# Kernel optimization log

Measured on AMD Instinct MI355X. Metric: run time of the kernel, lower is better.

The kernel has to match this reference:

```python
import jax, jax.numpy as jnp
import numpy as np

N_NODES = 100000
NEG_SLOPE = 0.2  # PyG GATConv default


def gat_conv(x, src, dst, W, a_src, a_dst, n_nodes):
    """One PyG-style GATConv (with self-loops already appended to src/dst).
    x: [N, Fin], W: [Fin, H*C], a_src/a_dst: [H, C]. Returns [N, H, C]."""
    H, C = a_src.shape
    h = (x @ W).reshape(-1, H, C)                      # [N, H, C]
    s_src = jnp.einsum('nhc,hc->nh', h, a_src)         # [N, H]
    s_dst = jnp.einsum('nhc,hc->nh', h, a_dst)         # [N, H]
    e = jax.nn.leaky_relu(s_src[src] + s_dst[dst], NEG_SLOPE)  # [E, H]
    # segment softmax over incoming edges of each destination node
    e_max = jax.ops.segment_max(e, dst, num_segments=n_nodes)  # [N, H]
    e_exp = jnp.exp(e - e_max[dst])
    denom = jax.ops.segment_sum(e_exp, dst, num_segments=n_nodes)
    alpha = e_exp / (denom[dst] + 1e-16)               # [E, H]
    msg = h[src] * alpha[:, :, None]                   # [E, H, C]
    return jax.ops.segment_sum(msg, dst, num_segments=n_nodes)  # [N, H, C]


def setup_inputs() -> dict:
    key = jax.random.key(0)
    ks = jax.random.split(key, 10)
    in_dim, hidden, heads, out_dim = 128, 32, 4, 32
    N, E = N_NODES, 1600000
    x = jax.random.normal(ks[0], (N, in_dim), dtype=jnp.float32)
    edge_index = jax.random.randint(ks[1], (2, E), 0, N, dtype=jnp.int64)
    s = 0.1
    return {
        'x': x,
        'edge_index': edge_index,
        'W1': s * jax.random.normal(ks[2], (in_dim, heads * hidden), dtype=jnp.float32),
        'a_src1': s * jax.random.normal(ks[3], (heads, hidden), dtype=jnp.float32),
        'a_dst1': s * jax.random.normal(ks[4], (heads, hidden), dtype=jnp.float32),
        'b1': jnp.zeros((heads * hidden,), dtype=jnp.float32),
        'W2': s * jax.random.normal(ks[5], (heads * hidden, out_dim), dtype=jnp.float32),
        'a_src2': s * jax.random.normal(ks[6], (1, out_dim), dtype=jnp.float32),
        'a_dst2': s * jax.random.normal(ks[7], (1, out_dim), dtype=jnp.float32),
        'b2': jnp.zeros((out_dim,), dtype=jnp.float32),
    }


def reference(x, edge_index, W1, a_src1, a_dst1, b1, W2, a_src2, a_dst2, b2):
    N = x.shape[0]
    loops = jnp.arange(N, dtype=edge_index.dtype)
    src = jnp.concatenate([edge_index[0], loops])  # PyG adds self-loops
    dst = jnp.concatenate([edge_index[1], loops])
    h1 = gat_conv(x, src, dst, W1, a_src1, a_dst1, N)      # [N, H, C]
    h1 = jax.nn.elu(h1.reshape(N, -1) + b1)                # concat heads + bias, elu
    h2 = gat_conv(h1, src, dst, W2, a_src2, a_dst2, N)     # [N, 1, out]
    return h2.mean(axis=1) + b2                            # concat=False -> mean over heads
```

## Files before the change

kernel.cpp:

```cpp
#include <hip/hip_runtime.h>
#include <hip/hip_bf16.h>

#define NEG 0.2f
#define BK_SHIFT 9
#define BK_CAP 9216

typedef short short8 __attribute__((ext_vector_type(8)));
typedef float f32x4 __attribute__((ext_vector_type(4)));

__device__ __forceinline__ float lrelu(float x){ return x > 0.f ? x : NEG * x; }
__device__ __forceinline__ float elu_fast(float x){ return x > 0.f ? x : __expf(x) - 1.f; }
__device__ __forceinline__ unsigned short f2bf(float f){
  unsigned int u = __float_as_uint(f);
  unsigned int r = u + 0x7fffu + ((u >> 16) & 1u);
  return (unsigned short)(r >> 16);
}
__device__ __forceinline__ float bf2f(unsigned short u){
  return __uint_as_float(((unsigned int)u) << 16);
}
__device__ __forceinline__ float2 bfu2(unsigned int v){
  float2 r;
  r.x = __uint_as_float(v << 16);
  r.y = __uint_as_float(v & 0xffff0000u);
  return r;
}

#define EB_SRC_MASK 0x7fffffu

__global__ __launch_bounds__(512) void k_binA_packW(
    const int* __restrict__ src, const int* __restrict__ dst, int E,
    int* __restrict__ gcursor, unsigned int* __restrict__ ebuf,
    const float* __restrict__ W, unsigned short* __restrict__ Wp,
    const float* __restrict__ W2, unsigned short* __restrict__ Wp2, int nA){
  __shared__ int hist[256];
  __shared__ int base[256];
  int t = threadIdx.x;
  int bid = blockIdx.x;
  if (bid >= nA){
    int idx = (bid - nA) * 512 + t;
    if (idx < 16384){
      int n = idx >> 7, k = idx & 127;
      Wp[n * 128 + k] = f2bf(W[(size_t)k * 128 + n]);
    } else {
      int i2 = idx - 16384;
      int n = i2 >> 7, k = i2 & 127;
      Wp2[n * 128 + k] = f2bf(W2[(size_t)k * 32 + n]);
    }
    return;
  }
  if (t < 256) hist[t] = 0;
  __syncthreads();
  int e0 = bid * 4096;
  int dsr[8], ssr[8];
  #pragma unroll
  for (int j = 0; j < 8; j++){
    int e = e0 + j * 512 + t;
    if (e < E){
      dsr[j] = dst[e]; ssr[j] = src[e];
      atomicAdd(&hist[dsr[j] >> BK_SHIFT], 1);
    } else dsr[j] = -1;
  }
  __syncthreads();
  if (t < 256){
    int cnt = hist[t];
    if (cnt > 0) base[t] = atomicAdd(&gcursor[t], cnt);
    hist[t] = 0;
  }
  __syncthreads();
  #pragma unroll
  for (int j = 0; j < 8; j++){
    if (dsr[j] >= 0){
      int d = dsr[j]; int b = d >> BK_SHIFT;
      int loc = atomicAdd(&hist[b], 1);
      unsigned int dloc = (unsigned int)(d & ((1 << BK_SHIFT) - 1));
      ebuf[(size_t)b * BK_CAP + base[b] + loc] = (unsigned int)ssr[j] | (dloc << 23);
    }
  }
}

__global__ __launch_bounds__(256, 3) void k_csrC_gemm1(
    const unsigned int* __restrict__ ebuf, const int* __restrict__ gcount,
    int* __restrict__ rowp, int* __restrict__ csr, int N, int NBK, int total,
    const float* __restrict__ x, const unsigned short* __restrict__ Wp,
    const float* __restrict__ a_src, const float* __restrict__ a_dst,
    unsigned short* __restrict__ h_bf, float* __restrict__ ss, float* __restrict__ sd){
  __shared__ __align__(16) unsigned short Wt[128 * 136];
  __shared__ __align__(16) unsigned short Xb[64 * 136];
  int t = threadIdx.x;

  if (blockIdx.x < (unsigned)NBK){
    int* hist = (int*)Wt;
    int* psum = hist + 512;
    int* bsum = psum + 256;
    int b = blockIdx.x;
    int nbase = b << BK_SHIFT;
    int cnt = gcount[b];
    const unsigned int* eb = ebuf + (size_t)b * BK_CAP;
    hist[t] = 0; hist[t + 256] = 0;
    int bv = 0;
    {
      int nodes = 0;
      if (t < NBK){ int nb = N - (t << BK_SHIFT); nodes = nb > 512 ? 512 : nb; bv = gcount[t] + nodes; }
      bsum[t] = bv;
    }
    __syncthreads();
    for (int off = 1; off < 256; off <<= 1){
      int xv = (t >= off) ? bsum[t - off] : 0;
      __syncthreads();
      bsum[t] += xv;
      __syncthreads();
    }
    for (int i = t; i < cnt; i += 256)
      atomicAdd(&hist[eb[i] >> 23], 1);
    __syncthreads();
    int v0 = hist[2 * t], v1 = hist[2 * t + 1];
    int ps = v0 + v1;
    psum[t] = ps;
    __syncthreads();
    for (int off = 1; off < 256; off <<= 1){
      int xv = (t >= off) ? psum[t - off] : 0;
      __syncthreads();
      psum[t] += xv;
      __syncthreads();
    }
    {
      int eo = psum[t] - ps;
      int bb = (b == 0) ? 0 : bsum[b - 1];
      int n0 = 2 * t, n1 = 2 * t + 1;
      int r0 = bb + eo + n0;
      int r1 = bb + eo + v0 + n1;
      if (nbase + n0 < N) rowp[nbase + n0] = r0;
      if (nbase + n1 < N) rowp[nbase + n1] = r1;
      hist[n0] = r0; hist[n1] = r1;
    }
    if (b == 0 && t == 0) rowp[N] = total;
    __syncthreads();
    for (int i = t; i < cnt; i += 256){
      unsigned int e = eb[i];
      int pos = atomicAdd(&hist[e >> 23], 1);
      csr[pos] = (int)(e & EB_SRC_MASK);
    }
    __syncthreads();
    {
      int n0 = 2 * t, n1 = 2 * t + 1;
      if (nbase + n0 < N) csr[hist[n0]] = nbase + n0;
      if (nbase + n1 < N) csr[hist[n1]] = nbase + n1;
    }
    return;
  }

  int rb = (blockIdx.x - NBK) * 64;

  #pragma unroll
  for (int j = 0; j < 8; j++){
    int fi = j * 256 + t;
    int n = fi >> 4, ch = fi & 15;
    *(uint4*)&Wt[n * 136 + ch * 8] = *(const uint4*)&Wp[n * 128 + ch * 8];
  }
  #pragma unroll
  for (int j = 0; j < 8; j++){
    int fi = j * 256 + t;
    int row = fi >> 5, k4 = (fi & 31) * 4;
    int gr = rb + row;
    float4 v = make_float4(0.f, 0.f, 0.f, 0.f);
    if (gr < N) v = *(const float4*)&x[(size_t)gr * 128 + k4];
    uint2 pk;
    pk.x = ((unsigned)f2bf(v.y) << 16) | f2bf(v.x);
    pk.y = ((unsigned)f2bf(v.w) << 16) | f2bf(v.z);
    *(uint2*)&Xb[row * 136 + k4] = pk;
  }
  __syncthreads();

  int w = t >> 6, l = t & 63;
  int m = l & 15, quad = l >> 4;
  f32x4 acc[8];
  #pragma unroll
  for (int ct = 0; ct < 8; ct++) acc[ct] = (f32x4){0.f, 0.f, 0.f, 0.f};

  #pragma unroll
  for (int kc = 0; kc < 4; kc++){
    short8 a = *(const short8*)&Xb[(w * 16 + m) * 136 + kc * 32 + quad * 8];
    #pragma unroll
    for (int ct = 0; ct < 8; ct++){
      short8 bfr = *(const short8*)&Wt[(ct * 16 + m) * 136 + kc * 32 + quad * 8];
      acc[ct] = __builtin_amdgcn_mfma_f32_16x16x32_bf16(a, bfr, acc[ct], 0, 0, 0);
    }
  }

  float as[8], ad[8];
  #pragma unroll
  for (int ct = 0; ct < 8; ct++){ as[ct] = a_src[ct * 16 + m]; ad[ct] = a_dst[ct * 16 + m]; }

  #pragma unroll
  for (int reg = 0; reg < 4; reg++){
    int gr = rb + w * 16 + quad * 4 + reg;
    bool ok = gr < N;
    if (ok){
      #pragma unroll
      for (int ct = 0; ct < 8; ct++)
        h_bf[(size_t)gr * 128 + ct * 16 + m] = f2bf(acc[ct][reg]);
    }
    #pragma unroll
    for (int hh = 0; hh < 4; hh++){
      float pss = acc[2*hh][reg] * as[2*hh] + acc[2*hh+1][reg] * as[2*hh+1];
      float pd = acc[2*hh][reg] * ad[2*hh] + acc[2*hh+1][reg] * ad[2*hh+1];
      pss += __shfl_xor(pss, 1, 16); pss += __shfl_xor(pss, 2, 16);
      pss += __shfl_xor(pss, 4, 16); pss += __shfl_xor(pss, 8, 16);
      pd += __shfl_xor(pd, 1, 16); pd += __shfl_xor(pd, 2, 16);
      pd += __shfl_xor(pd, 4, 16); pd += __shfl_xor(pd, 8, 16);
      if (m == 0 && ok){ ss[(size_t)gr * 4 + hh] = pss; sd[(size_t)gr * 4 + hh] = pd; }
    }
  }
}

__global__ __launch_bounds__(256) void k_agg1(
    const int* __restrict__ row_ptr, const int* __restrict__ csr_src,
    const float* __restrict__ ss, const float* __restrict__ sdst,
    const unsigned short* __restrict__ hb,
    unsigned int* __restrict__ out1_bf, int N){
  int n = blockIdx.x * 4 + (threadIdx.x >> 6);
  if (n >= N) return;
  int l = threadIdx.x & 63;
  int q  = (l & 7) + ((l >> 5) << 3);
  int hh = (l >> 3) & 3;
  int slot = l >> 4;
  int c = l & 15;
  int hd = c >> 2;
  float sdw = sdst[(size_t)n * 4 + hh];
  int beg = row_ptr[n], end = row_ptr[n + 1];

  float acc[8] = {0.f,0.f,0.f,0.f,0.f,0.f,0.f,0.f};
  float swacc = 0.f;

  int e = beg;
  int remaining = end - beg;
  int qc = q < remaining ? q : 0;
  int sj = csr_src[e + qc];
  float sv = ss[(size_t)sj * 4 + hh];

  while (remaining > 0){
    int cur = remaining > 16 ? 16 : remaining;
    float wv = (q < cur) ? __expf(lrelu(sv + sdw)) : 0.f;
    swacc += wv;
    int sjc = sj;
    int rn = remaining - 16;
    if (rn > 0){
      int qn = q < rn ? q : 0;
      sj = csr_src[e + 16 + qn];
      sv = ss[(size_t)sj * 4 + hh];
    }
    #pragma unroll
    for (int p = 0; p < 4; p++){
      int base_p = ((p & 1) << 2) + ((p >> 1) << 3);
      if (base_p < cur){
        int sl = ((p & 1) << 2) + slot + ((p >> 1) << 5);
        int s  = __shfl(sjc, sl, 64);
        float w = __shfl(wv, sl + (hd << 3), 64);
        uint4 u = *(const uint4*)&hb[(size_t)s * 128 + (c << 3)];
        float2 f0 = bfu2(u.x), f1 = bfu2(u.y), f2 = bfu2(u.z), f3 = bfu2(u.w);
        acc[0] += w * f0.x; acc[1] += w * f0.y;
        acc[2] += w * f1.x; acc[3] += w * f1.y;
        acc[4] += w * f2.x; acc[5] += w * f2.y;
        acc[6] += w * f3.x; acc[7] += w * f3.y;
      }
    }
    e += 16; remaining = rn;
  }

  #pragma unroll
  for (int i = 0; i < 8; i++){
    acc[i] += __shfl_xor(acc[i], 16, 64);
    acc[i] += __shfl_xor(acc[i], 32, 64);
  }
  swacc += __shfl_xor(swacc, 1, 64);
  swacc += __shfl_xor(swacc, 2, 64);
  swacc += __shfl_xor(swacc, 4, 64);
  swacc += __shfl_xor(swacc, 32, 64);
  float sw = __shfl(swacc, hd << 3, 64);
  float inv = 1.f / (sw + 1e-16f);
  if (slot == 0){
    unsigned int o0 = ((unsigned)f2bf(acc[1] * inv) << 16) | f2bf(acc[0] * inv);
    unsigned int o1 = ((unsigned)f2bf(acc[3] * inv) << 16) | f2bf(acc[2] * inv);
    unsigned int o2 = ((unsigned)f2bf(acc[5] * inv) << 16) | f2bf(acc[4] * inv);
    unsigned int o3 = ((unsigned)f2bf(acc[7] * inv) << 16) | f2bf(acc[6] * inv);
    uint4 o; o.x = o0; o.y = o1; o.z = o2; o.w = o3;
    *(uint4*)&out1_bf[(size_t)n * 64 + (c << 2)] = o;
  }
}

__global__ __launch_bounds__(256) void k_gemm2m(
    const unsigned int* __restrict__ out1_bf, const float* __restrict__ b1,
    const unsigned short* __restrict__ Wp2,
    const float* __restrict__ a_src, const float* __restrict__ a_dst,
    unsigned short* __restrict__ h2_bf, float* __restrict__ ss2, float* __restrict__ sd2, int N){
  __shared__ __align__(16) unsigned short Wt[32 * 136];
  __shared__ __align__(16) unsigned short Xb[128 * 136];
  int t = threadIdx.x;
  int rb = blockIdx.x * 128;

  #pragma unroll
  for (int j = 0; j < 2; j++){
    int fi = j * 256 + t;
    int n = fi >> 4, ch = fi & 15;
    *(uint4*)&Wt[n * 136 + ch * 8] = *(const uint4*)&Wp2[n * 128 + ch * 8];
  }
  #pragma unroll
  for (int j = 0; j < 8; j++){
    int fi = j * 256 + t;
    int row = fi >> 4, qq = fi & 15;
    int gr = rb + row;
    uint4 o = make_uint4(0u, 0u, 0u, 0u);
    if (gr < N){
      uint4 u = *(const uint4*)&out1_bf[(size_t)gr * 64 + qq * 4];
      float4 bva = *(const float4*)&b1[qq * 8];
      float4 bvb = *(const float4*)&b1[qq * 8 + 4];
      float v0 = elu_fast(bf2f((unsigned short)(u.x & 0xffff)) + bva.x);
      float v1 = elu_fast(bf2f((unsigned short)(u.x >> 16))    + bva.y);
      float v2 = elu_fast(bf2f((unsigned short)(u.y & 0xffff)) + bva.z);
      float v3 = elu_fast(bf2f((unsigned short)(u.y >> 16))    + bva.w);
      float v4 = elu_fast(bf2f((unsigned short)(u.z & 0xffff)) + bvb.x);
      float v5 = elu_fast(bf2f((unsigned short)(u.z >> 16))    + bvb.y);
      float v6 = elu_fast(bf2f((unsigned short)(u.w & 0xffff)) + bvb.z);
      float v7 = elu_fast(bf2f((unsigned short)(u.w >> 16))    + bvb.w);
      o.x = ((unsigned)f2bf(v1) << 16) | f2bf(v0);
      o.y = ((unsigned)f2bf(v3) << 16) | f2bf(v2);
      o.z = ((unsigned)f2bf(v5) << 16) | f2bf(v4);
      o.w = ((unsigned)f2bf(v7) << 16) | f2bf(v6);
    }
    *(uint4*)&Xb[row * 136 + qq * 8] = o;
  }
  __syncthreads();

  int w = t >> 6, l = t & 63;
  int m = l & 15, quad = l >> 4;
  f32x4 acc[2][2];
  #pragma unroll
  for (int rg = 0; rg < 2; rg++){
    acc[rg][0] = (f32x4){0.f, 0.f, 0.f, 0.f};
    acc[rg][1] = (f32x4){0.f, 0.f, 0.f, 0.f};
  }

  #pragma unroll
  for (int kc = 0; kc < 4; kc++){
    #pragma unroll
    for (int ct = 0; ct < 2; ct++){
      short8 bfr = *(const short8*)&Wt[(ct * 16 + m) * 136 + kc * 32 + quad * 8];
      #pragma unroll
      for (int rg = 0; rg < 2; rg++){
        short8 a = *(const short8*)&Xb[(rg * 64 + w * 16 + m) * 136 + kc * 32 + quad * 8];
        acc[rg][ct] = __builtin_amdgcn_mfma_f32_16x16x32_bf16(a, bfr, acc[rg][ct], 0, 0, 0);
      }
    }
  }

  float as0 = a_src[m], as1 = a_src[16 + m];
  float ad0 = a_dst[m], ad1 = a_dst[16 + m];

  #pragma unroll
  for (int rg = 0; rg < 2; rg++){
    #pragma unroll
    for (int reg = 0; reg < 4; reg++){
      int gr = rb + rg * 64 + w * 16 + quad * 4 + reg;
      bool ok = gr < N;
      if (ok){
        h2_bf[(size_t)gr * 32 + m]      = f2bf(acc[rg][0][reg]);
        h2_bf[(size_t)gr * 32 + 16 + m] = f2bf(acc[rg][1][reg]);
      }
      float ps = acc[rg][0][reg] * as0 + acc[rg][1][reg] * as1;
      float pd = acc[rg][0][reg] * ad0 + acc[rg][1][reg] * ad1;
      ps += __shfl_xor(ps, 1, 16); ps += __shfl_xor(ps, 2, 16);
      ps += __shfl_xor(ps, 4, 16); ps += __shfl_xor(ps, 8, 16);
      pd += __shfl_xor(pd, 1, 16); pd += __shfl_xor(pd, 2, 16);
      pd += __shfl_xor(pd, 4, 16); pd += __shfl_xor(pd, 8, 16);
      if (m == 0 && ok){ ss2[gr] = ps; sd2[gr] = pd; }
    }
  }
}

__global__ __launch_bounds__(256) void k_agg2(
    const int* __restrict__ row_ptr, const int* __restrict__ csr_src,
    const float* __restrict__ ss2, const float* __restrict__ sd2,
    const unsigned short* __restrict__ h2bf, const float* __restrict__ b2,
    float* __restrict__ out, int N){
  int n = blockIdx.x * 4 + (threadIdx.x >> 6);
  if (n >= N) return;
  int l = threadIdx.x & 63;
  int q = l & 31;
  int slot = l >> 2;
  int ch4 = l & 3;
  float sdv = sd2[n];
  int beg = row_ptr[n], end = row_ptr[n + 1];

  float acc[8] = {0.f,0.f,0.f,0.f,0.f,0.f,0.f,0.f};
  float swacc = 0.f;

  int e = beg;
  int remaining = end - beg;
  int qc = q < remaining ? q : 0;
  int sj = csr_src[e + qc];
  float sv = ss2[sj];

  while (remaining > 0){
    int cur = remaining > 32 ? 32 : remaining;
    float wv = (q < cur) ? __expf(lrelu(sv + sdv)) : 0.f;
    swacc += wv;
    int sjc = sj; float wvc = wv;
    int rn = remaining - 32;
    if (rn > 0){
      int qn = q < rn ? q : 0;
      sj = csr_src[e + 32 + qn];
      sv = ss2[sj];
    }
    {
      int s  = __shfl(sjc, slot, 64);
      float w = __shfl(wvc, slot, 64);
      if (slot < cur){
        uint4 u = *(const uint4*)&h2bf[(size_t)s * 32 + (ch4 << 3)];
        float2 f0 = bfu2(u.x), f1 = bfu2(u.y), f2 = bfu2(u.z), f3 = bfu2(u.w);
        acc[0] += w * f0.x; acc[1] += w * f0.y;
        acc[2] += w * f1.x; acc[3] += w * f1.y;
        acc[4] += w * f2.x; acc[5] += w * f2.y;
        acc[6] += w * f3.x; acc[7] += w * f3.y;
      }
    }
    if (cur > 16){
      int s  = __shfl(sjc, 16 + slot, 64);
      float w = __shfl(wvc, 16 + slot, 64);
      if (16 + slot < cur){
        uint4 u = *(const uint4*)&h2bf[(size_t)s * 32 + (ch4 << 3)];
        float2 f0 = bfu2(u.x), f1 = bfu2(u.y), f2 = bfu2(u.z), f3 = bfu2(u.w);
        acc[0] += w * f0.x; acc[1] += w * f0.y;
        acc[2] += w * f1.x; acc[3] += w * f1.y;
        acc[4] += w * f2.x; acc[5] += w * f2.y;
        acc[6] += w * f3.x; acc[7] += w * f3.y;
      }
    }
    e += 32; remaining = rn;
  }

  #pragma unroll
  for (int i = 0; i < 8; i++){
    acc[i] += __shfl_xor(acc[i], 4, 64);
    acc[i] += __shfl_xor(acc[i], 8, 64);
    acc[i] += __shfl_xor(acc[i], 16, 64);
    acc[i] += __shfl_xor(acc[i], 32, 64);
  }
  swacc += __shfl_xor(swacc, 1, 64);
  swacc += __shfl_xor(swacc, 2, 64);
  swacc += __shfl_xor(swacc, 4, 64);
  swacc += __shfl_xor(swacc, 8, 64);
  swacc += __shfl_xor(swacc, 16, 64);
  float inv = 1.f / (swacc + 1e-16f);
  if (slot == 0){
    float4 bva = *(const float4*)&b2[(ch4 << 3)];
    float4 bvb = *(const float4*)&b2[(ch4 << 3) + 4];
    float4 oa, ob;
    oa.x = acc[0] * inv + bva.x; oa.y = acc[1] * inv + bva.y;
    oa.z = acc[2] * inv + bva.z; oa.w = acc[3] * inv + bva.w;
    ob.x = acc[4] * inv + bvb.x; ob.y = acc[5] * inv + bvb.y;
    ob.z = acc[6] * inv + bvb.z; ob.w = acc[7] * inv + bvb.w;
    *(float4*)&out[(size_t)n * 32 + (ch4 << 3)] = oa;
    *(float4*)&out[(size_t)n * 32 + (ch4 << 3) + 4] = ob;
  }
}

extern "C" void kernel_launch(void* const* d_in, const int* in_sizes, int n_in,
                              void* d_out, int out_size, void* d_ws, size_t ws_size,
                              hipStream_t stream) {
  const float* x      = (const float*)d_in[0];
  const int*   ei     = (const int*)  d_in[1];
  const float* W1     = (const float*)d_in[2];
  const float* a_src1 = (const float*)d_in[3];
  const float* a_dst1 = (const float*)d_in[4];
  const float* b1     = (const float*)d_in[5];
  const float* W2     = (const float*)d_in[6];
  const float* a_src2 = (const float*)d_in[7];
  const float* a_dst2 = (const float*)d_in[8];
  const float* b2     = (const float*)d_in[9];
  float* out = (float*)d_out;

  int N = in_sizes[0] / 128;
  int E = in_sizes[1] / 2;
  const int* srcp = ei;
  const int* dstp = ei + E;
  int total = E + N;
  int NBK = (N + 511) >> 9;

  char* p = (char*)d_ws;
  auto alloc = [&](size_t bytes) -> void* {
    void* r = (void*)p; p += (bytes + 255) & ~(size_t)255; return r;
  };
  unsigned short* h_bf    = (unsigned short*)alloc((size_t)N * 128 * 2);
  unsigned int*   out1_bf = (unsigned int*)alloc((size_t)N * 64 * 4);
  unsigned short* h2_bf   = (unsigned short*)alloc((size_t)N * 32 * 2);
  unsigned short* Wp      = (unsigned short*)alloc(128 * 128 * 2);
  unsigned short* Wp2     = (unsigned short*)alloc(32 * 128 * 2);
  float* ss1  = (float*)alloc((size_t)N * 4 * 4);
  float* sd1  = (float*)alloc((size_t)N * 4 * 4);
  float* ss2  = (float*)alloc((size_t)N * 4);
  float* sd2  = (float*)alloc((size_t)N * 4);
  int* rowp   = (int*)alloc((size_t)(N + 1) * 4);
  int* csr    = (int*)alloc((size_t)total * 4);
  int* gcur   = (int*)alloc(256 * 4);
  unsigned int* ebuf = (unsigned int*)out1_bf;
  (void)ws_size; (void)n_in; (void)out_size;

  int nA = (E + 4095) / 4096;
  int nG = (N + 63) / 64;
  int nG2 = (N + 127) / 128;

  hipMemsetAsync(gcur, 0, 256 * 4, stream);
  k_binA_packW<<<nA + 40, 512, 0, stream>>>(srcp, dstp, E, gcur, ebuf, W1, Wp, W2, Wp2, nA);
  k_csrC_gemm1<<<NBK + nG, 256, 0, stream>>>(ebuf, gcur, rowp, csr, N, NBK, total,
                                             x, Wp, a_src1, a_dst1, h_bf, ss1, sd1);
  k_agg1<<<(N + 3) / 4, 256, 0, stream>>>(rowp, csr, ss1, sd1, h_bf, out1_bf, N);
  k_gemm2m<<<nG2, 256, 0, stream>>>(out1_bf, b1, Wp2, a_src2, a_dst2, h2_bf, ss2, sd2, N);
  k_agg2<<<(N + 3) / 4, 256, 0, stream>>>(rowp, csr, ss2, sd2, h2_bf, b2, out, N);
}
```

Before: 292.3 us.

## Compute per-node degrees globally and scatter CSR in a separate parallel kernel

```diff
diff --git a/kernel.cpp b/kernel.cpp
--- a/kernel.cpp
+++ b/kernel.cpp
@@ -29,7 +29,7 @@
 
 __global__ __launch_bounds__(512) void k_binA_packW(
     const int* __restrict__ src, const int* __restrict__ dst, int E,
-    int* __restrict__ gcursor, unsigned int* __restrict__ ebuf,
+    int* __restrict__ gcursor, int* __restrict__ deg, unsigned int* __restrict__ ebuf,
     const float* __restrict__ W, unsigned short* __restrict__ Wp,
     const float* __restrict__ W2, unsigned short* __restrict__ Wp2, int nA){
   __shared__ int hist[256];
@@ -58,6 +58,7 @@
     if (e < E){
       dsr[j] = dst[e]; ssr[j] = src[e];
       atomicAdd(&hist[dsr[j] >> BK_SHIFT], 1);
+      atomicAdd(&deg[dsr[j]], 1);
     } else dsr[j] = -1;
   }
   __syncthreads();
@@ -78,9 +79,10 @@
   }
 }
 
-__global__ __launch_bounds__(256, 3) void k_csrC_gemm1(
-    const unsigned int* __restrict__ ebuf, const int* __restrict__ gcount,
-    int* __restrict__ rowp, int* __restrict__ csr, int N, int NBK, int total,
+__global__ __launch_bounds__(256, 3) void k_scan_gemm1(
+    const int* __restrict__ gcount, const int* __restrict__ deg,
+    int* __restrict__ rowp, int* __restrict__ cur, int* __restrict__ csr,
+    int N, int NBK, int total,
     const float* __restrict__ x, const unsigned short* __restrict__ Wp,
     const float* __restrict__ a_src, const float* __restrict__ a_dst,
     unsigned short* __restrict__ h_bf, float* __restrict__ ss, float* __restrict__ sd){
@@ -89,63 +91,36 @@
   int t = threadIdx.x;
 
   if (blockIdx.x < (unsigned)NBK){
-    int* hist = (int*)Wt;
-    int* psum = hist + 512;
+    int* psum = (int*)Wt;
     int* bsum = psum + 256;
     int b = blockIdx.x;
     int nbase = b << BK_SHIFT;
-    int cnt = gcount[b];
-    const unsigned int* eb = ebuf + (size_t)b * BK_CAP;
-    hist[t] = 0; hist[t + 256] = 0;
     int bv = 0;
     {
       int nodes = 0;
       if (t < NBK){ int nb = N - (t << BK_SHIFT); nodes = nb > 512 ? 512 : nb; bv = gcount[t] + nodes; }
       bsum[t] = bv;
     }
-    __syncthreads();
-    for (int off = 1; off < 256; off <<= 1){
-      int xv = (t >= off) ? bsum[t - off] : 0;
-      __syncthreads();
-      bsum[t] += xv;
-      __syncthreads();
-    }
-    for (int i = t; i < cnt; i += 256)
-      atomicAdd(&hist[eb[i] >> 23], 1);
-    __syncthreads();
-    int v0 = hist[2 * t], v1 = hist[2 * t + 1];
-    int ps = v0 + v1;
+    int n0 = nbase + 2 * t, n1 = nbase + 2 * t + 1;
+    int d0 = (n0 < N) ? deg[n0] : 0;
+    int d1 = (n1 < N) ? deg[n1] : 0;
+    int ps = d0 + d1;
     psum[t] = ps;
     __syncthreads();
     for (int off = 1; off < 256; off <<= 1){
-      int xv = (t >= off) ? psum[t - off] : 0;
+      int xa = (t >= off) ? bsum[t - off] : 0;
+      int xb = (t >= off) ? psum[t - off] : 0;
       __syncthreads();
-      psum[t] += xv;
+      bsum[t] += xa; psum[t] += xb;
       __syncthreads();
     }
-    {
-      int eo = psum[t] - ps;
-      int bb = (b == 0) ? 0 : bsum[b - 1];
-      int n0 = 2 * t, n1 = 2 * t + 1;
-      int r0 = bb + eo + n0;
-      int r1 = bb + eo + v0 + n1;
-      if (nbase + n0 < N) rowp[nbase + n0] = r0;
-      if (nbase + n1 < N) rowp[nbase + n1] = r1;
-      hist[n0] = r0; hist[n1] = r1;
-    }
+    int eo = psum[t] - ps;
+    int bb = (b == 0) ? 0 : bsum[b - 1];
+    int r0 = bb + eo + 2 * t;
+    int r1 = bb + eo + d0 + 2 * t + 1;
+    if (n0 < N){ rowp[n0] = r0; cur[n0] = r0; csr[r0 + d0] = n0; }
+    if (n1 < N){ rowp[n1] = r1; cur[n1] = r1; csr[r1 + d1] = n1; }
     if (b == 0 && t == 0) rowp[N] = total;
-    __syncthreads();
-    for (int i = t; i < cnt; i += 256){
-      unsigned int e = eb[i];
-      int pos = atomicAdd(&hist[e >> 23], 1);
-      csr[pos] = (int)(e & EB_SRC_MASK);
-    }
-    __syncthreads();
-    {
-      int n0 = 2 * t, n1 = 2 * t + 1;
-      if (nbase + n0 < N) csr[hist[n0]] = nbase + n0;
-      if (nbase + n1 < N) csr[hist[n1]] = nbase + n1;
-    }
     return;
   }
 
@@ -210,6 +185,21 @@
       pd += __shfl_xor(pd, 4, 16); pd += __shfl_xor(pd, 8, 16);
       if (m == 0 && ok){ ss[(size_t)gr * 4 + hh] = pss; sd[(size_t)gr * 4 + hh] = pd; }
     }
+  }
+}
+
+__global__ __launch_bounds__(256) void k_place(
+    const unsigned int* __restrict__ ebuf, const int* __restrict__ gcount,
+    int* __restrict__ cur, int* __restrict__ csr){
+  int b = blockIdx.x >> 2;
+  int h = blockIdx.x & 3;
+  int cnt = gcount[b];
+  int nbase = b << BK_SHIFT;
+  const unsigned int* eb = ebuf + (size_t)b * BK_CAP;
+  for (int i = h * 256 + threadIdx.x; i < cnt; i += 1024){
+    unsigned int e = eb[i];
+    int pos = atomicAdd(&cur[nbase + (int)(e >> 23)], 1);
+    csr[pos] = (int)(e & EB_SRC_MASK);
   }
 }
 
@@ -239,8 +229,8 @@
   float sv = ss[(size_t)sj * 4 + hh];
 
   while (remaining > 0){
-    int cur = remaining > 16 ? 16 : remaining;
-    float wv = (q < cur) ? __expf(lrelu(sv + sdw)) : 0.f;
+    int cur_ = remaining > 16 ? 16 : remaining;
+    float wv = (q < cur_) ? __expf(lrelu(sv + sdw)) : 0.f;
     swacc += wv;
     int sjc = sj;
     int rn = remaining - 16;
@@ -252,7 +242,7 @@
     #pragma unroll
     for (int p = 0; p < 4; p++){
       int base_p = ((p & 1) << 2) + ((p >> 1) << 3);
-      if (base_p < cur){
+      if (base_p < cur_){
         int sl = ((p & 1) << 2) + slot + ((p >> 1) << 5);
         int s  = __shfl(sjc, sl, 64);
         float w = __shfl(wv, sl + (hd << 3), 64);
@@ -401,8 +391,8 @@
   float sv = ss2[sj];
 
   while (remaining > 0){
-    int cur = remaining > 32 ? 32 : remaining;
-    float wv = (q < cur) ? __expf(lrelu(sv + sdv)) : 0.f;
+    int cur_ = remaining > 32 ? 32 : remaining;
+    float wv = (q < cur_) ? __expf(lrelu(sv + sdv)) : 0.f;
     swacc += wv;
     int sjc = sj; float wvc = wv;
     int rn = remaining - 32;
@@ -414,7 +404,7 @@
     {
       int s  = __shfl(sjc, slot, 64);
       float w = __shfl(wvc, slot, 64);
-      if (slot < cur){
+      if (slot < cur_){
         uint4 u = *(const uint4*)&h2bf[(size_t)s * 32 + (ch4 << 3)];
         float2 f0 = bfu2(u.x), f1 = bfu2(u.y), f2 = bfu2(u.z), f3 = bfu2(u.w);
         acc[0] += w * f0.x; acc[1] += w * f0.y;
@@ -423,10 +413,10 @@
         acc[6] += w * f3.x; acc[7] += w * f3.y;
       }
     }
-    if (cur > 16){
+    if (cur_ > 16){
       int s  = __shfl(sjc, 16 + slot, 64);
       float w = __shfl(wvc, 16 + slot, 64);
-      if (16 + slot < cur){
+      if (16 + slot < cur_){
         uint4 u = *(const uint4*)&h2bf[(size_t)s * 32 + (ch4 << 3)];
         float2 f0 = bfu2(u.x), f1 = bfu2(u.y), f2 = bfu2(u.z), f3 = bfu2(u.w);
         acc[0] += w * f0.x; acc[1] += w * f0.y;
@@ -502,6 +492,8 @@
   int* rowp   = (int*)alloc((size_t)(N + 1) * 4);
   int* csr    = (int*)alloc((size_t)total * 4);
   int* gcur   = (int*)alloc(256 * 4);
+  int* deg    = (int*)alloc((size_t)N * 4);
+  int* cur    = (int*)alloc((size_t)N * 4);
   unsigned int* ebuf = (unsigned int*)out1_bf;
   (void)ws_size; (void)n_in; (void)out_size;
 
@@ -509,10 +501,11 @@
   int nG = (N + 63) / 64;
   int nG2 = (N + 127) / 128;
 
-  hipMemsetAsync(gcur, 0, 256 * 4, stream);
-  k_binA_packW<<<nA + 40, 512, 0, stream>>>(srcp, dstp, E, gcur, ebuf, W1, Wp, W2, Wp2, nA);
-  k_csrC_gemm1<<<NBK + nG, 256, 0, stream>>>(ebuf, gcur, rowp, csr, N, NBK, total,
+  hipMemsetAsync(gcur, 0, (size_t)(256 + N) * 4, stream);
+  k_binA_packW<<<nA + 40, 512, 0, stream>>>(srcp, dstp, E, gcur, deg, ebuf, W1, Wp, W2, Wp2, nA);
+  k_scan_gemm1<<<NBK + nG, 256, 0, stream>>>(gcur, deg, rowp, cur, csr, N, NBK, total,
                                              x, Wp, a_src1, a_dst1, h_bf, ss1, sd1);
+  k_place<<<NBK * 4, 256, 0, stream>>>(ebuf, gcur, cur, csr);
   k_agg1<<<(N + 3) / 4, 256, 0, stream>>>(rowp, csr, ss1, sd1, h_bf, out1_bf, N);
   k_gemm2m<<<nG2, 256, 0, stream>>>(out1_bf, b1, Wp2, a_src2, a_dst2, h2_bf, ss2, sd2, N);
   k_agg2<<<(N + 3) / 4, 256, 0, stream>>>(rowp, csr, ss2, sd2, h2_bf, b2, out, N);
```

Result: slower. 394.5 us (+35.0%).
